# Kernel optimization log

Measured on AMD Instinct MI355X. Metric: run time of the kernel, lower is better.

The kernel has to match this reference:

```python
import jax, jax.numpy as jnp
import numpy as np

P = 16            # num_patches = 224 // 14
T = P * P         # patches per image (256)
K = 5             # top-k templates
SIM_THR = 0.05
PATCH_THR = 2.0


def _idx2loc(idx):
    # flat patch index -> (w, h) float location, matching convert_index2location
    return jnp.stack([(idx % P).astype(jnp.float32), (idx // P).astype(jnp.float32)], axis=-1)


def setup_inputs() -> dict:
    key = jax.random.key(0)
    k1, k2, k3, k4 = jax.random.split(key, 4)
    B, N, C = 8, 32, 768
    src_feats = jax.random.normal(k1, (B, N, C, P, P), dtype=jnp.float32)
    tar_feat = jax.random.normal(k2, (B, C, P, P), dtype=jnp.float32)
    src_masks = (jax.random.uniform(k3, (B, N, P, P)) > 0.3).astype(jnp.float32)
    tar_mask = (jax.random.uniform(k4, (B, P, P)) > 0.3).astype(jnp.float32)
    return {"src_feats": src_feats, "tar_feat": tar_feat,
            "src_masks": src_masks, "tar_mask": tar_mask}


def reference(src_feats, tar_feat, src_masks, tar_mask):
    B, N, C = src_feats.shape[:3]
    # masks are already at feature resolution -> interpolate is identity; flatten
    tarm = tar_mask.reshape(B, T)                                   # (B, T)
    srcm = src_masks.reshape(B, N, T)                               # (B, N, T)
    # L2-normalize features over channel dim (F.normalize)
    tf = tar_feat / jnp.clip(jnp.linalg.norm(tar_feat, axis=1, keepdims=True), 1e-12)
    tf = tf.reshape(B, C, T)                                        # (B, C, T)
    sf = src_feats / jnp.clip(jnp.linalg.norm(src_feats, axis=2, keepdims=True), 1e-12)
    sf = sf.reshape(B, N, C, T)                                     # (B, N, C, S)
    # dense cosine similarity, masked, then thresholded to 0
    sim = jnp.einsum('bct,bncs->bnts', tf, sf)                      # (B, N, T, S)
    sim = sim * srcm[:, :, None, :] * tarm[:, None, :, None]
    sim = jnp.where(sim < SIM_THR, 0.0, sim)
    # dual nearest-neighbor search ('tar2src' direction)
    score_t2s = sim.max(axis=3)                                     # (B, N, T)
    idx_t2s = sim.argmax(axis=3).astype(jnp.int32)
    score_s2t = sim.max(axis=2)                                     # (B, N, S)
    idx_s2t = sim.argmax(axis=2).astype(jnp.int32)
    mask_sim = score_t2s >= SIM_THR
    # cycle consistency: tar -> src -> tar
    idx_s2s = jnp.take_along_axis(idx_s2t, idx_t2s, axis=2)         # (B, N, T)
    dist = jnp.linalg.norm(_idx2loc(idx_s2s) - _idx2loc(jnp.arange(T))[None, None], axis=-1)
    sim_s2s = jnp.take_along_axis(score_s2t, idx_t2s, axis=2)
    mask_cycle = (dist <= PATCH_THR) & (sim_s2s >= SIM_THR)
    # non-zero / in-mask filtering
    mask_t2s = jnp.take_along_axis(srcm, idx_t2s, axis=2)           # (B, N, T)
    mask_nz = tarm[:, None, :] * mask_t2s * (idx_s2t != 0) * (idx_t2s != 0)
    mask_all = (mask_sim & mask_cycle) * mask_nz                    # (B, N, T) float
    match_counts = mask_all.sum(axis=2)                             # (B, N)
    sim_avg = jnp.where(match_counts > 0,
                        (score_t2s * mask_all).sum(axis=2) / float(T), 0.0)
    # top-k template selection
    score_src, id_src = jax.lax.top_k(sim_avg, K)                   # (B, K)
    sel = lambda a: jnp.take_along_axis(a, id_src[:, :, None], axis=1)
    pred_mask = sel(mask_all)                                       # (B, K, T)
    score_pts = sel(score_t2s)                                      # (B, K, T)
    src_loc = _idx2loc(sel(idx_t2s)).astype(jnp.int32)              # (B, K, T, 2)
    # format_prediction: -1 outside mask, (w, h) coords inside
    grid = _idx2loc(jnp.arange(T)).astype(jnp.int32)                # (T, 2)
    nz = (pred_mask != 0)[..., None]
    tar_pts = jnp.where(nz, grid[None, None], -1)                   # (B, K, T, 2)
    src_pts = jnp.where(nz, src_loc, -1)                            # (B, K, T, 2)
    return id_src, score_src, score_pts, tar_pts, src_pts, match_counts
```

## Files before the change

kernel.cpp:

```cpp
#include <hip/hip_runtime.h>

#define T_PATCH 256
#define C_DIM   768
#define N_B     8
#define N_N     32

typedef unsigned short u16;
typedef u16   u16x8  __attribute__((ext_vector_type(8)));
typedef short s16x8  __attribute__((ext_vector_type(8)));
typedef float f32x16 __attribute__((ext_vector_type(16)));

__device__ __forceinline__ unsigned rne16(unsigned u) {
    return (u + 0x7fffu + ((u >> 16) & 1u)) >> 16;
}

__launch_bounds__(512, 2)
__global__ void sim_kernel(const float* __restrict__ src_feats,
                           const float* __restrict__ tar_feat,
                           const float* __restrict__ src_masks,
                           const float* __restrict__ tar_mask,
                           float* __restrict__ w_score,
                           float* __restrict__ w_mall,
                           float* __restrict__ w_savg,
                           int*   __restrict__ w_idx,
                           float* __restrict__ out) {
    __shared__ __align__(16) u16 A0[2][2][256][8];
    __shared__ __align__(16) u16 A1[2][2][256][8];
    __shared__ __align__(16) u16 A2[2][2][256][8];
    __shared__ __align__(16) u16 B0[2][2][256][8];
    __shared__ __align__(16) u16 B1[2][2][256][8];
    __shared__ __align__(16) u16 B2[2][2][256][8];
    __shared__ float sqT[512], sqS[512];
    __shared__ float rowv[2][256];  __shared__ int rowi[2][256];
    __shared__ float colv[4][256];  __shared__ int coli[4][256];
    __shared__ float sc_t2s[256];   __shared__ int ix_t2s[256];
    __shared__ float sc_s2t[256];   __shared__ int ix_s2t[256];
    __shared__ float invT[256], invS[256], tm[256], sm[256];
    __shared__ float red[8];

    int bn  = blockIdx.x;
    int b   = bn >> 5;
    int tid = threadIdx.x;
    int lane = tid & 63, w = tid >> 6;
    int wm = w >> 1, wn = w & 1;
    int h = lane >> 5, l5 = lane & 31;
    int tS = tid & 255, g = tid >> 8;

    const float* tb = tar_feat + (size_t)b  * C_DIM * T_PATCH;
    const float* sb = src_feats + (size_t)bn * C_DIM * T_PATCH;

    if (tid < 256) {
        tm[tid] = tar_mask[b * T_PATCH + tid];
        sm[tid] = src_masks[bn * T_PATCH + tid];
    }

    f32x16 acc[2][4];
    #pragma unroll
    for (int i = 0; i < 2; ++i)
        #pragma unroll
        for (int j = 0; j < 4; ++j) acc[i][j] = (f32x16)0.0f;

    float tss = 0.f, sss = 0.f;
    float xv[8], yv[8];
    #pragma unroll
    for (int j = 0; j < 8; ++j) {
        xv[j] = tb[(g * 8 + j) * T_PATCH + tS];
        yv[j] = sb[(g * 8 + j) * T_PATCH + tS];
    }

    int buf = 0;
    for (int c0 = 0; c0 < C_DIM; c0 += 16, buf ^= 1) {
        __syncthreads();
        u16x8 t0v, t1v, t2v, s0v, s1v, s2v;
        #pragma unroll
        for (int j = 0; j < 8; ++j) {
            float x = xv[j];
            unsigned u0 = rne16(__float_as_uint(x));
            float f0 = __uint_as_float(u0 << 16);
            float r1 = x - f0;
            unsigned u1 = rne16(__float_as_uint(r1));
            float f1 = __uint_as_float(u1 << 16);
            float r2 = r1 - f1;
            t0v[j] = (u16)u0;
            t1v[j] = (u16)u1;
            t2v[j] = (u16)(__float_as_uint(r2) >> 16);
            tss = fmaf(x, x, tss);
            float y = yv[j];
            unsigned v0 = rne16(__float_as_uint(y));
            float g0 = __uint_as_float(v0 << 16);
            float q1 = y - g0;
            unsigned v1 = rne16(__float_as_uint(q1));
            float g1 = __uint_as_float(v1 << 16);
            float q2 = q1 - g1;
            s0v[j] = (u16)v0;
            s1v[j] = (u16)v1;
            s2v[j] = (u16)(__float_as_uint(q2) >> 16);
            sss = fmaf(y, y, sss);
        }
        *(u16x8*)&A0[buf][g][tS][0] = t0v;
        *(u16x8*)&A1[buf][g][tS][0] = t1v;
        *(u16x8*)&A2[buf][g][tS][0] = t2v;
        *(u16x8*)&B0[buf][g][tS][0] = s0v;
        *(u16x8*)&B1[buf][g][tS][0] = s1v;
        *(u16x8*)&B2[buf][g][tS][0] = s2v;
        int c1 = c0 + 16;
        if (c1 < C_DIM) {
            #pragma unroll
            for (int j = 0; j < 8; ++j) {
                xv[j] = tb[(c1 + g * 8 + j) * T_PATCH + tS];
                yv[j] = sb[(c1 + g * 8 + j) * T_PATCH + tS];
            }
        }
        __syncthreads();
        s16x8 a0[2], a1[2], a2[2];
        #pragma unroll
        for (int i = 0; i < 2; ++i) {
            int row = wm * 64 + i * 32 + l5;
            a0[i] = *(const s16x8*)&A0[buf][h][row][0];
            a1[i] = *(const s16x8*)&A1[buf][h][row][0];
            a2[i] = *(const s16x8*)&A2[buf][h][row][0];
        }
        #pragma unroll
        for (int j = 0; j < 4; ++j) {
            int col = wn * 128 + j * 32 + l5;
            s16x8 b0 = *(const s16x8*)&B0[buf][h][col][0];
            s16x8 b1 = *(const s16x8*)&B1[buf][h][col][0];
            s16x8 b2 = *(const s16x8*)&B2[buf][h][col][0];
            #pragma unroll
            for (int i = 0; i < 2; ++i) {
                acc[i][j] = __builtin_amdgcn_mfma_f32_32x32x16_bf16(a0[i], b0, acc[i][j], 0, 0, 0);
                acc[i][j] = __builtin_amdgcn_mfma_f32_32x32x16_bf16(a0[i], b1, acc[i][j], 0, 0, 0);
                acc[i][j] = __builtin_amdgcn_mfma_f32_32x32x16_bf16(a1[i], b0, acc[i][j], 0, 0, 0);
                acc[i][j] = __builtin_amdgcn_mfma_f32_32x32x16_bf16(a1[i], b1, acc[i][j], 0, 0, 0);
                acc[i][j] = __builtin_amdgcn_mfma_f32_32x32x16_bf16(a0[i], b2, acc[i][j], 0, 0, 0);
                acc[i][j] = __builtin_amdgcn_mfma_f32_32x32x16_bf16(a2[i], b0, acc[i][j], 0, 0, 0);
            }
        }
    }

    sqT[g * 256 + tS] = tss;
    sqS[g * 256 + tS] = sss;
    __syncthreads();
    if (tid < 256) {
        float nt = sqrtf(sqT[tid] + sqT[256 + tid]);
        invT[tid] = (tm[tid] != 0.f) ? 1.f / fmaxf(nt, 1e-12f) : 0.f;
        float ns = sqrtf(sqS[tid] + sqS[256 + tid]);
        invS[tid] = (sm[tid] != 0.f) ? 1.f / fmaxf(ns, 1e-12f) : 0.f;
    }
    __syncthreads();

    float isv[4];
    #pragma unroll
    for (int j = 0; j < 4; ++j) isv[j] = invS[wn * 128 + j * 32 + l5];

    float cbv[4]; int cbi[4];
    #pragma unroll
    for (int j = 0; j < 4; ++j) { cbv[j] = -1.f; cbi[j] = 0; }

    #pragma unroll
    for (int i = 0; i < 2; ++i) {
        #pragma unroll
        for (int r = 0; r < 16; ++r) {
            int trow = wm * 64 + i * 32 + (r & 3) + 8 * (r >> 2) + 4 * h;
            float it = invT[trow];
            float v[4];
            #pragma unroll
            for (int j = 0; j < 4; ++j) {
                float x = acc[i][j][r] * it * isv[j];
                v[j] = (x >= 0.05f) ? x : 0.f;
            }
            float bv = -1.f; int bi = 0;
            #pragma unroll
            for (int j = 0; j < 4; ++j) {
                int s = wn * 128 + j * 32 + l5;
                if (v[j] > bv) { bv = v[j]; bi = s; }
            }
            #pragma unroll
            for (int off = 1; off < 32; off <<= 1) {
                float ov = __shfl_xor(bv, off, 64);
                int   oi = __shfl_xor(bi, off, 64);
                if (ov > bv || (ov == bv && oi < bi)) { bv = ov; bi = oi; }
            }
            if (l5 == 0) { rowv[wn][trow] = bv; rowi[wn][trow] = bi; }
            #pragma unroll
            for (int j = 0; j < 4; ++j) {
                if (v[j] > cbv[j]) { cbv[j] = v[j]; cbi[j] = trow; }
            }
        }
    }
    #pragma unroll
    for (int j = 0; j < 4; ++j) {
        float bv = cbv[j]; int bi = cbi[j];
        float ov = __shfl_xor(bv, 32, 64);
        int   oi = __shfl_xor(bi, 32, 64);
        if (ov > bv || (ov == bv && oi < bi)) { bv = ov; bi = oi; }
        if (h == 0) { colv[wm][wn * 128 + j * 32 + l5] = bv; coli[wm][wn * 128 + j * 32 + l5] = bi; }
    }
    __syncthreads();
    if (tid < 256) {
        float bv = rowv[0][tid]; int bi = rowi[0][tid];
        float ov = rowv[1][tid]; int oi = rowi[1][tid];
        if (ov > bv || (ov == bv && oi < bi)) { bv = ov; bi = oi; }
        sc_t2s[tid] = bv; ix_t2s[tid] = bi;
        bv = colv[0][tid]; bi = coli[0][tid];
        #pragma unroll
        for (int q = 1; q < 4; ++q) {
            ov = colv[q][tid]; oi = coli[q][tid];
            if (ov > bv || (ov == bv && oi < bi)) { bv = ov; bi = oi; }
        }
        sc_s2t[tid] = bv; ix_s2t[tid] = bi;
    }
    __syncthreads();

    float cnt = 0.f, svs = 0.f;
    if (tid < 256) {
        int t = tid;
        float st2s = sc_t2s[t];
        int   i    = ix_t2s[t];
        bool msim = st2s >= 0.05f;
        int is2s = ix_s2t[i];
        int dw = (is2s & 15) - (t & 15);
        int dh = (is2s >> 4) - (t >> 4);
        bool cyc = (dw * dw + dh * dh <= 4) && (sc_s2t[i] >= 0.05f);
        float mnz = tm[t] * sm[i] *
                    ((ix_s2t[t] != 0) ? 1.f : 0.f) *
                    ((i != 0) ? 1.f : 0.f);
        float mall = (msim && cyc) ? mnz : 0.f;
        w_score[bn * T_PATCH + t] = st2s;
        w_mall[bn * T_PATCH + t]  = mall;
        w_idx[bn * T_PATCH + t]   = i;
        cnt = mall;
        svs = st2s * mall;
    }
    #pragma unroll
    for (int off = 1; off < 64; off <<= 1) {
        cnt += __shfl_xor(cnt, off, 64);
        svs += __shfl_xor(svs, off, 64);
    }
    if (tid < 256 && (tid & 63) == 0) {
        red[(tid >> 6) * 2]     = cnt;
        red[(tid >> 6) * 2 + 1] = svs;
    }
    __syncthreads();
    if (tid == 0) {
        float c = red[0] + red[2] + red[4] + red[6];
        float s = red[1] + red[3] + red[5] + red[7];
        w_savg[bn] = (c > 0.f) ? (s * (1.f / 256.f)) : 0.f;
        out[51280 + bn] = c;
    }
}

__global__ void final_kernel(const float* __restrict__ w_score,
                             const float* __restrict__ w_mall,
                             const float* __restrict__ w_savg,
                             const int*   __restrict__ w_idx,
                             float* __restrict__ out) {
    int b = blockIdx.x, tid = threadIdx.x;
    __shared__ float savg[32];
    __shared__ int   topid[5];
    __shared__ float topv[5];
    if (tid < 32) savg[tid] = w_savg[b * 32 + tid];
    __syncthreads();
    if (tid == 0) {
        unsigned used = 0;
        for (int k = 0; k < 5; ++k) {
            float bv = -1e30f; int bi = 0;
            for (int n = 0; n < 32; ++n) {
                if (!((used >> n) & 1u) && savg[n] > bv) { bv = savg[n]; bi = n; }
            }
            used |= (1u << bi);
            topid[k] = bi; topv[k] = bv;
        }
    }
    __syncthreads();
    if (tid < 5) {
        out[b * 5 + tid]      = (float)topid[tid];
        out[40 + b * 5 + tid] = topv[tid];
    }
    int t = tid;
    for (int k = 0; k < 5; ++k) {
        int bn = b * 32 + topid[k];
        float sc = w_score[bn * 256 + t];
        float ma = w_mall[bn * 256 + t];
        int   ii = w_idx[bn * 256 + t];
        int o = (b * 5 + k) * 256 + t;
        out[80 + o] = sc;
        bool nz = (ma != 0.f);
        out[10320 + 2 * o]     = nz ? (float)(t & 15)  : -1.f;
        out[10320 + 2 * o + 1] = nz ? (float)(t >> 4)  : -1.f;
        out[30800 + 2 * o]     = nz ? (float)(ii & 15) : -1.f;
        out[30800 + 2 * o + 1] = nz ? (float)(ii >> 4) : -1.f;
    }
}

extern "C" void kernel_launch(void* const* d_in, const int* in_sizes, int n_in,
                              void* d_out, int out_size, void* d_ws, size_t ws_size,
                              hipStream_t stream) {
    const float* src_feats = (const float*)d_in[0];
    const float* tar_feat  = (const float*)d_in[1];
    const float* src_masks = (const float*)d_in[2];
    const float* tar_mask  = (const float*)d_in[3];
    float* out = (float*)d_out;

    float* ws      = (float*)d_ws;
    float* w_score = ws;
    float* w_mall  = w_score + 65536;
    float* w_savg  = w_mall + 65536;
    int*   w_idx   = (int*)(w_savg + 256);

    sim_kernel<<<N_B * N_N, 512, 0, stream>>>(src_feats, tar_feat, src_masks,
                                              tar_mask,
                                              w_score, w_mall, w_savg, w_idx, out);
    final_kernel<<<N_B, 256, 0, stream>>>(w_score, w_mall, w_savg, w_idx, out);
}
```

Measured before the change: 371.7 us.

## Precompute target bf16 split once and split sim kernel across source halves

```diff
diff --git a/kernel.cpp b/kernel.cpp
--- a/kernel.cpp
+++ b/kernel.cpp
@@ -2,6 +2,7 @@
 
 #define T_PATCH 256
 #define C_DIM   768
+#define NCH     48
 #define N_B     8
 #define N_N     32
 
@@ -14,118 +15,133 @@
     return (u + 0x7fffu + ((u >> 16) & 1u)) >> 16;
 }
 
-__launch_bounds__(512, 2)
+__device__ __forceinline__ void split3(float x, u16& o0, u16& o1, u16& o2) {
+    unsigned u0 = rne16(__float_as_uint(x));
+    float f0 = __uint_as_float(u0 << 16);
+    float r1 = x - f0;
+    unsigned u1 = rne16(__float_as_uint(r1));
+    float f1 = __uint_as_float(u1 << 16);
+    float r2 = r1 - f1;
+    o0 = (u16)u0; o1 = (u16)u1; o2 = (u16)(__float_as_uint(r2) >> 16);
+}
+
+__global__ void tar_split_kernel(const float* __restrict__ tar,
+                                 u16* __restrict__ tS0, u16* __restrict__ tS1,
+                                 u16* __restrict__ tS2, float* __restrict__ partT) {
+    int blk = blockIdx.x;
+    int b = blk / NCH, c = blk - b * NCH;
+    int tid = threadIdx.x;
+    int g = tid >> 8, t = tid & 255;
+    const float* tb = tar + (size_t)b * C_DIM * T_PATCH;
+    float ss = 0.f;
+    u16x8 v0, v1, v2;
+    #pragma unroll
+    for (int j = 0; j < 8; ++j) {
+        float x = tb[(c * 16 + g * 8 + j) * T_PATCH + t];
+        u16 a, bb, cc;
+        split3(x, a, bb, cc);
+        v0[j] = a; v1[j] = bb; v2[j] = cc;
+        ss = fmaf(x, x, ss);
+    }
+    size_t off = ((size_t)blk * 512 + tid) * 8;
+    *(u16x8*)(tS0 + off) = v0;
+    *(u16x8*)(tS1 + off) = v1;
+    *(u16x8*)(tS2 + off) = v2;
+    __shared__ float sq[512];
+    sq[tid] = ss;
+    __syncthreads();
+    if (tid < 256) partT[blk * 256 + tid] = sq[tid] + sq[tid + 256];
+}
+
+__global__ void invt_kernel(const float* __restrict__ partT,
+                            const float* __restrict__ tar_mask,
+                            float* __restrict__ w_invT) {
+    int b = blockIdx.x, t = threadIdx.x;
+    float s = 0.f;
+    for (int c = 0; c < NCH; ++c) s += partT[(b * NCH + c) * 256 + t];
+    float tm = tar_mask[b * 256 + t];
+    w_invT[b * 256 + t] = (tm != 0.f) ? 1.f / fmaxf(sqrtf(s), 1e-12f) : 0.f;
+}
+
+__launch_bounds__(512, 4)
 __global__ void sim_kernel(const float* __restrict__ src_feats,
-                           const float* __restrict__ tar_feat,
+                           const u16* __restrict__ tS0, const u16* __restrict__ tS1,
+                           const u16* __restrict__ tS2,
+                           const float* __restrict__ w_invT,
                            const float* __restrict__ src_masks,
-                           const float* __restrict__ tar_mask,
-                           float* __restrict__ w_score,
-                           float* __restrict__ w_mall,
-                           float* __restrict__ w_savg,
-                           int*   __restrict__ w_idx,
-                           float* __restrict__ out) {
-    __shared__ __align__(16) u16 A0[2][2][256][8];
-    __shared__ __align__(16) u16 A1[2][2][256][8];
-    __shared__ __align__(16) u16 A2[2][2][256][8];
-    __shared__ __align__(16) u16 B0[2][2][256][8];
-    __shared__ __align__(16) u16 B1[2][2][256][8];
-    __shared__ __align__(16) u16 B2[2][2][256][8];
-    __shared__ float sqT[512], sqS[512];
-    __shared__ float rowv[2][256];  __shared__ int rowi[2][256];
-    __shared__ float colv[4][256];  __shared__ int coli[4][256];
-    __shared__ float sc_t2s[256];   __shared__ int ix_t2s[256];
-    __shared__ float sc_s2t[256];   __shared__ int ix_s2t[256];
-    __shared__ float invT[256], invS[256], tm[256], sm[256];
-    __shared__ float red[8];
-
-    int bn  = blockIdx.x;
-    int b   = bn >> 5;
+                           float* __restrict__ w_rowv, int* __restrict__ w_rowi,
+                           float* __restrict__ w_s2tv, int* __restrict__ w_s2ti) {
+    __shared__ __align__(16) u16 A0[2][256][8], A1[2][256][8], A2[2][256][8];
+    __shared__ __align__(16) u16 B0[2][128][8], B1[2][128][8], B2[2][128][8];
+    __shared__ float sqS[2][128];
+    __shared__ float rowv[2][256]; __shared__ int rowi[2][256];
+    __shared__ float colv[4][128]; __shared__ int coli[4][128];
+    __shared__ float invT[256], invS[128];
+
+    int bh = blockIdx.x;
+    int bn = bh >> 1, half = bh & 1;
+    int b  = bn >> 5;
     int tid = threadIdx.x;
     int lane = tid & 63, w = tid >> 6;
     int wm = w >> 1, wn = w & 1;
     int h = lane >> 5, l5 = lane & 31;
-    int tS = tid & 255, g = tid >> 8;
-
-    const float* tb = tar_feat + (size_t)b  * C_DIM * T_PATCH;
-    const float* sb = src_feats + (size_t)bn * C_DIM * T_PATCH;
-
-    if (tid < 256) {
-        tm[tid] = tar_mask[b * T_PATCH + tid];
-        sm[tid] = src_masks[bn * T_PATCH + tid];
-    }
-
-    f32x16 acc[2][4];
+    int colB = tid & 127, gB = (tid >> 7) & 1;
+
+    const float* sb = src_feats + (size_t)bn * C_DIM * T_PATCH + half * 128;
+
+    if (tid < 256) invT[tid] = w_invT[b * 256 + tid];
+
+    f32x16 acc[2][2];
     #pragma unroll
     for (int i = 0; i < 2; ++i)
         #pragma unroll
-        for (int j = 0; j < 4; ++j) acc[i][j] = (f32x16)0.0f;
-
-    float tss = 0.f, sss = 0.f;
-    float xv[8], yv[8];
-    #pragma unroll
-    for (int j = 0; j < 8; ++j) {
-        xv[j] = tb[(g * 8 + j) * T_PATCH + tS];
-        yv[j] = sb[(g * 8 + j) * T_PATCH + tS];
-    }
-
-    int buf = 0;
-    for (int c0 = 0; c0 < C_DIM; c0 += 16, buf ^= 1) {
+        for (int j = 0; j < 2; ++j) acc[i][j] = (f32x16)0.0f;
+
+    float sss = 0.f;
+
+    for (int c = 0; c < NCH; ++c) {
+        float yv[8];
+        if (tid < 256) {
+            #pragma unroll
+            for (int j = 0; j < 8; ++j)
+                yv[j] = sb[(c * 16 + gB * 8 + j) * T_PATCH + colB];
+        }
+        size_t aoff = (((size_t)(b * NCH + c)) * 512 + tid) * 8;
+        u16x8 a0v = *(const u16x8*)(tS0 + aoff);
+        u16x8 a1v = *(const u16x8*)(tS1 + aoff);
+        u16x8 a2v = *(const u16x8*)(tS2 + aoff);
         __syncthreads();
-        u16x8 t0v, t1v, t2v, s0v, s1v, s2v;
-        #pragma unroll
-        for (int j = 0; j < 8; ++j) {
-            float x = xv[j];
-            unsigned u0 = rne16(__float_as_uint(x));
-            float f0 = __uint_as_float(u0 << 16);
-            float r1 = x - f0;
-            unsigned u1 = rne16(__float_as_uint(r1));
-            float f1 = __uint_as_float(u1 << 16);
-            float r2 = r1 - f1;
-            t0v[j] = (u16)u0;
-            t1v[j] = (u16)u1;
-            t2v[j] = (u16)(__float_as_uint(r2) >> 16);
-            tss = fmaf(x, x, tss);
-            float y = yv[j];
-            unsigned v0 = rne16(__float_as_uint(y));
-            float g0 = __uint_as_float(v0 << 16);
-            float q1 = y - g0;
-            unsigned v1 = rne16(__float_as_uint(q1));
-            float g1 = __uint_as_float(v1 << 16);
-            float q2 = q1 - g1;
-            s0v[j] = (u16)v0;
-            s1v[j] = (u16)v1;
-            s2v[j] = (u16)(__float_as_uint(q2) >> 16);
-            sss = fmaf(y, y, sss);
-        }
-        *(u16x8*)&A0[buf][g][tS][0] = t0v;
-        *(u16x8*)&A1[buf][g][tS][0] = t1v;
-        *(u16x8*)&A2[buf][g][tS][0] = t2v;
-        *(u16x8*)&B0[buf][g][tS][0] = s0v;
-        *(u16x8*)&B1[buf][g][tS][0] = s1v;
-        *(u16x8*)&B2[buf][g][tS][0] = s2v;
-        int c1 = c0 + 16;
-        if (c1 < C_DIM) {
+        ((u16x8*)A0)[tid] = a0v;
+        ((u16x8*)A1)[tid] = a1v;
+        ((u16x8*)A2)[tid] = a2v;
+        if (tid < 256) {
+            u16x8 b0v, b1v, b2v;
             #pragma unroll
             for (int j = 0; j < 8; ++j) {
-                xv[j] = tb[(c1 + g * 8 + j) * T_PATCH + tS];
-                yv[j] = sb[(c1 + g * 8 + j) * T_PATCH + tS];
-            }
+                u16 a, bb, cc;
+                split3(yv[j], a, bb, cc);
+                b0v[j] = a; b1v[j] = bb; b2v[j] = cc;
+                sss = fmaf(yv[j], yv[j], sss);
+            }
+            ((u16x8*)B0)[tid] = b0v;
+            ((u16x8*)B1)[tid] = b1v;
+            ((u16x8*)B2)[tid] = b2v;
         }
         __syncthreads();
         s16x8 a0[2], a1[2], a2[2];
         #pragma unroll
         for (int i = 0; i < 2; ++i) {
             int row = wm * 64 + i * 32 + l5;
-            a0[i] = *(const s16x8*)&A0[buf][h][row][0];
-            a1[i] = *(const s16x8*)&A1[buf][h][row][0];
-            a2[i] = *(const s16x8*)&A2[buf][h][row][0];
-        }
-        #pragma unroll
-        for (int j = 0; j < 4; ++j) {
-            int col = wn * 128 + j * 32 + l5;
-            s16x8 b0 = *(const s16x8*)&B0[buf][h][col][0];
-            s16x8 b1 = *(const s16x8*)&B1[buf][h][col][0];
-            s16x8 b2 = *(const s16x8*)&B2[buf][h][col][0];
+            a0[i] = *(const s16x8*)&A0[h][row][0];
+            a1[i] = *(const s16x8*)&A1[h][row][0];
+            a2[i] = *(const s16x8*)&A2[h][row][0];
+        }
+        #pragma unroll
+        for (int j = 0; j < 2; ++j) {
+            int cl = wn * 64 + j * 32 + l5;
+            s16x8 b0 = *(const s16x8*)&B0[h][cl][0];
+            s16x8 b1 = *(const s16x8*)&B1[h][cl][0];
+            s16x8 b2 = *(const s16x8*)&B2[h][cl][0];
             #pragma unroll
             for (int i = 0; i < 2; ++i) {
                 acc[i][j] = __builtin_amdgcn_mfma_f32_32x32x16_bf16(a0[i], b0, acc[i][j], 0, 0, 0);
@@ -138,24 +154,25 @@
         }
     }
 
-    sqT[g * 256 + tS] = tss;
-    sqS[g * 256 + tS] = sss;
-    __syncthreads();
-    if (tid < 256) {
-        float nt = sqrtf(sqT[tid] + sqT[256 + tid]);
-        invT[tid] = (tm[tid] != 0.f) ? 1.f / fmaxf(nt, 1e-12f) : 0.f;
-        float ns = sqrtf(sqS[tid] + sqS[256 + tid]);
-        invS[tid] = (sm[tid] != 0.f) ? 1.f / fmaxf(ns, 1e-12f) : 0.f;
-    }
-    __syncthreads();
-
-    float isv[4];
-    #pragma unroll
-    for (int j = 0; j < 4; ++j) isv[j] = invS[wn * 128 + j * 32 + l5];
-
-    float cbv[4]; int cbi[4];
-    #pragma unroll
-    for (int j = 0; j < 4; ++j) { cbv[j] = -1.f; cbi[j] = 0; }
+    __syncthreads();
+    if (tid < 256) ((float*)sqS)[tid] = sss;
+    __syncthreads();
+    if (tid < 128) {
+        float ns = sqrtf(sqS[0][tid] + sqS[1][tid]);
+        float smv = src_masks[bn * 256 + half * 128 + tid];
+        invS[tid] = (smv != 0.f) ? 1.f / fmaxf(ns, 1e-12f) : 0.f;
+    }
+    __syncthreads();
+
+    float isv[2]; int sgl[2];
+    #pragma unroll
+    for (int j = 0; j < 2; ++j) {
+        isv[j] = invS[wn * 64 + j * 32 + l5];
+        sgl[j] = half * 128 + wn * 64 + j * 32 + l5;
+    }
+    float cbv[2]; int cbi[2];
+    #pragma unroll
+    for (int j = 0; j < 2; ++j) { cbv[j] = -1.f; cbi[j] = 0; }
 
     #pragma unroll
     for (int i = 0; i < 2; ++i) {
@@ -163,18 +180,16 @@
         for (int r = 0; r < 16; ++r) {
             int trow = wm * 64 + i * 32 + (r & 3) + 8 * (r >> 2) + 4 * h;
             float it = invT[trow];
-            float v[4];
-            #pragma unroll
-            for (int j = 0; j < 4; ++j) {
+            float v[2];
+            #pragma unroll
+            for (int j = 0; j < 2; ++j) {
                 float x = acc[i][j][r] * it * isv[j];
                 v[j] = (x >= 0.05f) ? x : 0.f;
             }
             float bv = -1.f; int bi = 0;
             #pragma unroll
-            for (int j = 0; j < 4; ++j) {
-                int s = wn * 128 + j * 32 + l5;
-                if (v[j] > bv) { bv = v[j]; bi = s; }
-            }
+            for (int j = 0; j < 2; ++j)
+                if (v[j] > bv) { bv = v[j]; bi = sgl[j]; }
             #pragma unroll
             for (int off = 1; off < 32; off <<= 1) {
                 float ov = __shfl_xor(bv, off, 64);
@@ -183,66 +198,84 @@
             }
             if (l5 == 0) { rowv[wn][trow] = bv; rowi[wn][trow] = bi; }
             #pragma unroll
-            for (int j = 0; j < 4; ++j) {
+            for (int j = 0; j < 2; ++j)
                 if (v[j] > cbv[j]) { cbv[j] = v[j]; cbi[j] = trow; }
-            }
-        }
-    }
-    #pragma unroll
-    for (int j = 0; j < 4; ++j) {
+        }
+    }
+    #pragma unroll
+    for (int j = 0; j < 2; ++j) {
         float bv = cbv[j]; int bi = cbi[j];
         float ov = __shfl_xor(bv, 32, 64);
         int   oi = __shfl_xor(bi, 32, 64);
         if (ov > bv || (ov == bv && oi < bi)) { bv = ov; bi = oi; }
-        if (h == 0) { colv[wm][wn * 128 + j * 32 + l5] = bv; coli[wm][wn * 128 + j * 32 + l5] = bi; }
+        if (h == 0) { colv[wm][wn * 64 + j * 32 + l5] = bv; coli[wm][wn * 64 + j * 32 + l5] = bi; }
     }
     __syncthreads();
     if (tid < 256) {
-        float bv = rowv[0][tid]; int bi = rowi[0][tid];
-        float ov = rowv[1][tid]; int oi = rowi[1][tid];
-        if (ov > bv || (ov == bv && oi < bi)) { bv = ov; bi = oi; }
-        sc_t2s[tid] = bv; ix_t2s[tid] = bi;
-        bv = colv[0][tid]; bi = coli[0][tid];
+        float v0 = rowv[0][tid]; int i0 = rowi[0][tid];
+        float v1 = rowv[1][tid]; int i1 = rowi[1][tid];
+        if (v1 > v0 || (v1 == v0 && i1 < i0)) { v0 = v1; i0 = i1; }
+        w_rowv[bh * 256 + tid] = v0;
+        w_rowi[bh * 256 + tid] = i0;
+    }
+    if (tid < 128) {
+        float bv = colv[0][tid]; int bi = coli[0][tid];
         #pragma unroll
         for (int q = 1; q < 4; ++q) {
-            ov = colv[q][tid]; oi = coli[q][tid];
+            float ov = colv[q][tid]; int oi = coli[q][tid];
             if (ov > bv || (ov == bv && oi < bi)) { bv = ov; bi = oi; }
         }
-        sc_s2t[tid] = bv; ix_s2t[tid] = bi;
-    }
-    __syncthreads();
-
-    float cnt = 0.f, svs = 0.f;
-    if (tid < 256) {
-        int t = tid;
-        float st2s = sc_t2s[t];
-        int   i    = ix_t2s[t];
-        bool msim = st2s >= 0.05f;
-        int is2s = ix_s2t[i];
-        int dw = (is2s & 15) - (t & 15);
-        int dh = (is2s >> 4) - (t >> 4);
-        bool cyc = (dw * dw + dh * dh <= 4) && (sc_s2t[i] >= 0.05f);
-        float mnz = tm[t] * sm[i] *
-                    ((ix_s2t[t] != 0) ? 1.f : 0.f) *
-                    ((i != 0) ? 1.f : 0.f);
-        float mall = (msim && cyc) ? mnz : 0.f;
-        w_score[bn * T_PATCH + t] = st2s;
-        w_mall[bn * T_PATCH + t]  = mall;
-        w_idx[bn * T_PATCH + t]   = i;
-        cnt = mall;
-        svs = st2s * mall;
-    }
+        w_s2tv[bn * 256 + half * 128 + tid] = bv;
+        w_s2ti[bn * 256 + half * 128 + tid] = bi;
+    }
+}
+
+__global__ void combine_kernel(const float* __restrict__ w_rowv, const int* __restrict__ w_rowi,
+                               const float* __restrict__ w_s2tv, const int* __restrict__ w_s2ti,
+                               const float* __restrict__ src_masks, const float* __restrict__ tar_mask,
+                               float* __restrict__ w_score, float* __restrict__ w_mall,
+                               float* __restrict__ w_savg, int* __restrict__ w_idx,
+                               float* __restrict__ out) {
+    int bn = blockIdx.x; int b = bn >> 5; int t = threadIdx.x;
+    __shared__ float sc_s2t[256]; __shared__ int ix_s2t[256];
+    __shared__ float sm[256];
+    __shared__ float red[8];
+    sc_s2t[t] = w_s2tv[bn * 256 + t];
+    ix_s2t[t] = w_s2ti[bn * 256 + t];
+    sm[t]     = src_masks[bn * 256 + t];
+    float v0 = w_rowv[(bn * 2) * 256 + t];     int i0 = w_rowi[(bn * 2) * 256 + t];
+    float v1 = w_rowv[(bn * 2 + 1) * 256 + t]; int i1 = w_rowi[(bn * 2 + 1) * 256 + t];
+    float st2s; int i;
+    if (v1 > v0 || (v1 == v0 && i1 < i0)) { st2s = v1; i = i1; }
+    else                                  { st2s = v0; i = i0; }
+    float tmv = tar_mask[b * 256 + t];
+    __syncthreads();
+
+    bool msim = st2s >= 0.05f;
+    int is2s = ix_s2t[i];
+    int dw = (is2s & 15) - (t & 15);
+    int dh = (is2s >> 4) - (t >> 4);
+    bool cyc = (dw * dw + dh * dh <= 4) && (sc_s2t[i] >= 0.05f);
+    float mnz = tmv * sm[i] *
+                ((ix_s2t[t] != 0) ? 1.f : 0.f) *
+                ((i != 0) ? 1.f : 0.f);
+    float mall = (msim && cyc) ? mnz : 0.f;
+    w_score[bn * 256 + t] = st2s;
+    w_mall[bn * 256 + t]  = mall;
+    w_idx[bn * 256 + t]   = i;
+
+    float cnt = mall, svs = st2s * mall;
     #pragma unroll
     for (int off = 1; off < 64; off <<= 1) {
         cnt += __shfl_xor(cnt, off, 64);
         svs += __shfl_xor(svs, off, 64);
     }
-    if (tid < 256 && (tid & 63) == 0) {
-        red[(tid >> 6) * 2]     = cnt;
-        red[(tid >> 6) * 2 + 1] = svs;
-    }
-    __syncthreads();
-    if (tid == 0) {
+    if ((t & 63) == 0) {
+        red[(t >> 6) * 2]     = cnt;
+        red[(t >> 6) * 2 + 1] = svs;
+    }
+    __syncthreads();
+    if (t == 0) {
         float c = red[0] + red[2] + red[4] + red[6];
         float s = red[1] + red[3] + red[5] + red[7];
         w_savg[bn] = (c > 0.f) ? (s * (1.f / 256.f)) : 0.f;
@@ -302,14 +335,28 @@
     const float* tar_mask  = (const float*)d_in[3];
     float* out = (float*)d_out;
 
-    float* ws      = (float*)d_ws;
-    float* w_score = ws;
-    float* w_mall  = w_score + 65536;
-    float* w_savg  = w_mall + 65536;
+    const size_t PLANE = (size_t)N_B * NCH * 512 * 8;
+    u16* tS0 = (u16*)d_ws;
+    u16* tS1 = tS0 + PLANE;
+    u16* tS2 = tS1 + PLANE;
+    float* partT  = (float*)(tS2 + PLANE);
+    float* w_invT = partT + (size_t)N_B * NCH * 256;
+    float* w_rowv = w_invT + 2048;
+    int*   w_rowi = (int*)(w_rowv + 512 * 256);
+    float* w_s2tv = (float*)(w_rowi + 512 * 256);
+    int*   w_s2ti = (int*)(w_s2tv + 256 * 256);
+    float* w_score = (float*)(w_s2ti + 256 * 256);
+    float* w_mall  = w_score + 256 * 256;
+    float* w_savg  = w_mall + 256 * 256;
     int*   w_idx   = (int*)(w_savg + 256);
 
-    sim_kernel<<<N_B * N_N, 512, 0, stream>>>(src_feats, tar_feat, src_masks,
-                                              tar_mask,
-                                              w_score, w_mall, w_savg, w_idx, out);
+    tar_split_kernel<<<N_B * NCH, 512, 0, stream>>>(tar_feat, tS0, tS1, tS2, partT);
+    invt_kernel<<<N_B, 256, 0, stream>>>(partT, tar_mask, w_invT);
+    sim_kernel<<<N_B * N_N * 2, 512, 0, stream>>>(src_feats, tS0, tS1, tS2, w_invT,
+                                                  src_masks,
+                                                  w_rowv, w_rowi, w_s2tv, w_s2ti);
+    combine_kernel<<<N_B * N_N, 256, 0, stream>>>(w_rowv, w_rowi, w_s2tv, w_s2ti,
+                                                  src_masks, tar_mask,
+                                                  w_score, w_mall, w_savg, w_idx, out);
     final_kernel<<<N_B, 256, 0, stream>>>(w_score, w_mall, w_savg, w_idx, out);
 }
```

Result: no change. 366.9 us (-1.3%).
